# Kernel optimization log

Measured on AMD Instinct MI355X. Metric: run time of the kernel, lower is better.

The kernel has to match this reference:

```python
import jax, jax.numpy as jnp
import numpy as np

KH, KW = 3, 3
PAD = 1
STRIDE = 1


def dht1(x):
    # 1D Discrete Hartley Transform along last axis: Re(FFT) - Im(FFT)
    f = jnp.fft.fft(x, axis=-1)
    return f.real - f.imag


def dht2(x, fft_h, fft_w):
    # zero-pad trailing two dims up to (fft_h, fft_w), then DHT along w then h
    pad_h = fft_h - x.shape[-2]
    pad_w = fft_w - x.shape[-1]
    pads = [(0, 0)] * (x.ndim - 2) + [(0, pad_h), (0, pad_w)]
    x = jnp.pad(x, pads)
    x = dht1(x)
    x = jnp.swapaxes(dht1(jnp.swapaxes(x, -1, -2)), -1, -2)
    return x


def setup_inputs() -> dict:
    key = jax.random.key(0)
    k1, k2 = jax.random.split(key)
    x = jax.random.normal(k1, (8, 64, 128, 128), dtype=jnp.float32)
    weight = jax.random.normal(k2, (64, 64, KH, KW), dtype=jnp.float32)
    return {"x": x, "weight": weight}


def reference(x, weight):
    b, c_in, h, w = x.shape
    out_h = (h + 2 * PAD - KH) // STRIDE + 1
    out_w = (w + 2 * PAD - KW) // STRIDE + 1
    x_p = jnp.pad(x, ((0, 0), (0, 0), (PAD, PAD), (PAD, PAD)))
    fft_h = h + 2 * PAD + KH - 1
    fft_w = w + 2 * PAD + KW - 1

    x_ht = dht2(x_p, fft_h, fft_w)          # [B, Cin, fh, fw]
    w_ht = dht2(weight, fft_h, fft_w)        # [Cout, Cin, fh, fw]

    x_f = jnp.flip(x_ht, axis=(-2, -1))
    w_f = jnp.flip(w_ht, axis=(-2, -1))

    # Fused combine + sum over Cin: avoids [B,Cout,Cin,fh,fw] intermediates.
    t1 = jnp.einsum('bchw,ochw->bohw', x_ht, w_ht)
    t2 = jnp.einsum('bchw,ochw->bohw', x_ht, w_f)
    t3 = jnp.einsum('bchw,ochw->bohw', x_f, w_ht)
    t4 = jnp.einsum('bchw,ochw->bohw', x_f, w_f)
    out_ht = (t1 + t2 + t3 - t4) * 0.5

    # idht2 in the source applies only the 1/n scaling twice (no transform)
    output = out_ht / jnp.asarray(fft_h * fft_w, dtype=out_ht.dtype)
    return output[:, :, :out_h, :out_w]
```

## Files before the change

### kernel.cpp

```cpp
#include <hip/hip_runtime.h>
#include <hip/hip_fp16.h>


#define SCALE (0.5f / 17424.0f)

typedef __attribute__((ext_vector_type(8))) _Float16 f16x8;
typedef __attribute__((ext_vector_type(4))) _Float16 f16x4;
typedef __attribute__((ext_vector_type(4))) float    f32x4;

__global__ void build_tf16(_Float16* __restrict__ Tf) {
    const int u = blockIdx.x;
    const int i = threadIdx.x;
    float val = 0.f;
    if (u < 132) {
        const int m = (u * (i + 1)) % 132;
        const float step = 6.28318530717958647692f / 132.0f;
        float s, c;
        sincosf((float)m * step, &s, &c);
        val = c + s;
    }
    Tf[u * 128 + i] = (_Float16)val;
}

__global__ void build_cf(_Float16* __restrict__ cfT) {
    const int v = threadIdx.x;
    const float step = 6.28318530717958647692f / 132.0f;
    float s, c;
    _Float16 o[8];
    o[0] = (_Float16)1.0f; o[3] = (_Float16)1.0f;
    o[6] = (_Float16)0.0f; o[7] = (_Float16)0.0f;
    sincosf((float)((v * 1) % 132) * step, &s, &c);      o[1] = (_Float16)(c + s);
    sincosf((float)((v * 2) % 132) * step, &s, &c);      o[2] = (_Float16)(c + s);
    sincosf((float)(((v + 1) * 1) % 132) * step, &s, &c); o[4] = (_Float16)(c - s);
    sincosf((float)(((v + 1) * 2) % 132) * step, &s, &c); o[5] = (_Float16)(c - s);
    *(f16x8*)(cfT + v * 8) = *(f16x8*)o;
}

__global__ __launch_bounds__(256) void build_hgT(
    const float* __restrict__ w, _Float16* __restrict__ hgT)
{
    const int u = blockIdx.x;
    const float step = 6.28318530717958647692f / 132.0f;
    float a[3], ap[3];
    a[0] = 1.f; ap[0] = 1.f;
    #pragma unroll
    for (int i = 1; i < 3; ++i) {
        float s, c;
        sincosf((float)((u * i) % 132) * step, &s, &c);
        a[i] = c + s;
        sincosf((float)(((u + 1) * i) % 132) * step, &s, &c);
        ap[i] = c - s;
    }
    for (int it = 0; it < 16; ++it) {
        const int oc = it * 256 + threadIdx.x;
        const float* wp = w + (size_t)oc * 9;
        float w9[9];
        #pragma unroll
        for (int q = 0; q < 9; ++q) w9[q] = wp[q];
        #pragma unroll
        for (int j = 0; j < 3; ++j) {
            const float h = a[0]*w9[j] + a[1]*w9[3+j] + a[2]*w9[6+j];
            const float g = ap[0]*w9[j] + ap[1]*w9[3+j] + ap[2]*w9[6+j];
            hgT[((size_t)u * 6 + j)     * 4096 + oc] = (_Float16)h;
            hgT[((size_t)u * 6 + 3 + j) * 4096 + oc] = (_Float16)g;
        }
    }
}

__global__ __launch_bounds__(256, 2) void dht2_fused(
    const float* __restrict__ x, const _Float16* __restrict__ Tf,
    _Float16* __restrict__ X)
{
    const int bc = blockIdx.x;
    const int tid = threadIdx.x, wv = tid >> 6, lane = tid & 63;
    const int col = lane & 15, quad = lane >> 4;
    __shared__ _Float16 Tfl[144][136];
    __shared__ _Float16 Y1l[144][136];

    const float* xp = x + (size_t)bc * 16384;

    float4 xv[2][4][2];
    #pragma unroll
    for (int nt = 0; nt < 2; ++nt) {
        const int ic = (wv * 2 + nt) * 16 + col;
        #pragma unroll
        for (int kc = 0; kc < 4; ++kc) {
            const int k0 = kc * 32 + quad * 8;
            xv[nt][kc][0] = *(const float4*)(xp + ic * 128 + k0);
            xv[nt][kc][1] = *(const float4*)(xp + ic * 128 + k0 + 4);
        }
    }
    #pragma unroll
    for (int s = 0; s < 9; ++s) {
        const int idx = tid + 256 * s;
        const int row = idx >> 4;
        const int ce  = (idx & 15) * 8;
        *(f16x8*)&Tfl[row][ce] = *(const f16x8*)(Tf + (size_t)idx * 8);
    }
    f16x8 bfA[2][4];
    #pragma unroll
    for (int nt = 0; nt < 2; ++nt)
        #pragma unroll
        for (int kc = 0; kc < 4; ++kc) {
            f16x8 t;
            t[0] = (_Float16)xv[nt][kc][0].x; t[1] = (_Float16)xv[nt][kc][0].y;
            t[2] = (_Float16)xv[nt][kc][0].z; t[3] = (_Float16)xv[nt][kc][0].w;
            t[4] = (_Float16)xv[nt][kc][1].x; t[5] = (_Float16)xv[nt][kc][1].y;
            t[6] = (_Float16)xv[nt][kc][1].z; t[7] = (_Float16)xv[nt][kc][1].w;
            bfA[nt][kc] = t;
        }
    __syncthreads();

    f32x4 accA[2][9];
    #pragma unroll
    for (int nt = 0; nt < 2; ++nt)
        #pragma unroll
        for (int mt = 0; mt < 9; ++mt) accA[nt][mt] = (f32x4)0.f;
    #pragma unroll
    for (int kc = 0; kc < 4; ++kc) {
        const int k0 = kc * 32 + quad * 8;
        #pragma unroll
        for (int mt = 0; mt < 9; ++mt) {
            const f16x8 af = *(const f16x8*)&Tfl[mt * 16 + col][k0];
            accA[0][mt] = __builtin_amdgcn_mfma_f32_16x16x32_f16(af, bfA[0][kc], accA[0][mt], 0, 0, 0);
            accA[1][mt] = __builtin_amdgcn_mfma_f32_16x16x32_f16(af, bfA[1][kc], accA[1][mt], 0, 0, 0);
        }
    }
    #pragma unroll
    for (int nt = 0; nt < 2; ++nt) {
        const int ic = (wv * 2 + nt) * 16 + col;
        #pragma unroll
        for (int mt = 0; mt < 9; ++mt)
            #pragma unroll
            for (int r = 0; r < 4; ++r)
                Y1l[mt * 16 + quad * 4 + r][ic] = (_Float16)accA[nt][mt][r];
    }
    __syncthreads();

    f32x4 accB[3][9];
    #pragma unroll
    for (int t = 0; t < 3; ++t)
        #pragma unroll
        for (int mt = 0; mt < 9; ++mt) accB[t][mt] = (f32x4)0.f;
    #pragma unroll
    for (int kc = 0; kc < 4; ++kc) {
        const int k0 = kc * 32 + quad * 8;
        f16x8 af9[9];
        #pragma unroll
        for (int mt = 0; mt < 9; ++mt)
            af9[mt] = *(const f16x8*)&Tfl[mt * 16 + col][k0];
        #pragma unroll
        for (int t = 0; t < 3; ++t) {
            const int nt = wv + 4 * t;
            if (nt < 9) {
                const f16x8 bf = *(const f16x8*)&Y1l[nt * 16 + col][k0];
                #pragma unroll
                for (int mt = 0; mt < 9; ++mt)
                    accB[t][mt] = __builtin_amdgcn_mfma_f32_16x16x32_f16(af9[mt], bf, accB[t][mt], 0, 0, 0);
            }
        }
    }
    _Float16* Xp = X + (size_t)bc * 17424;
    #pragma unroll
    for (int t = 0; t < 3; ++t) {
        const int nt = wv + 4 * t;
        if (nt < 9) {
            const int vg = nt * 16 + col;
            if (vg < 132) {
                #pragma unroll
                for (int mt = 0; mt < 9; ++mt)
                    #pragma unroll
                    for (int r = 0; r < 4; ++r) {
                        const int u = mt * 16 + quad * 4 + r;
                        if (u < 132) Xp[u * 132 + vg] = (_Float16)accB[t][mt][r];
                    }
            }
        }
    }
}

__global__ __launch_bounds__(256) void combine_mfma(
    const _Float16* __restrict__ X, const _Float16* __restrict__ hgT,
    const _Float16* __restrict__ cfT, float* __restrict__ out)
{
    const int u = blockIdx.x;
    const int b = blockIdx.y;
    const int tid = threadIdx.x;
    const int wv = tid >> 6, lane = tid & 63;
    const int col = lane & 15, quad = lane >> 4;

    __shared__ _Float16 Ps[128][72];
    __shared__ _Float16 Ms[128][72];

    {
        const int c  = tid >> 2;
        const int vq = (tid & 3) * 32;
        const _Float16* rowd = X + (size_t)(b * 64 + c) * 17424 + (size_t)u * 132;
        const _Float16* rowm = X + (size_t)(b * 64 + c) * 17424 + (size_t)(131 - u) * 132;
        #pragma unroll
        for (int k = 0; k < 8; ++k) {
            const int v0 = vq + 4 * k;
            const f16x4 d = *(const f16x4*)(rowd + v0);
            const f16x4 m = *(const f16x4*)(rowm + (128 - v0));
            #pragma unroll
            for (int i = 0; i < 4; ++i) {
                Ps[v0 + i][c] = d[i] + m[3 - i];
                Ms[v0 + i][c] = d[i] - m[3 - i];
            }
        }
    }
    f16x8 cfv[8];
    #pragma unroll
    for (int nt = 0; nt < 8; ++nt)
        cfv[nt] = *(const f16x8*)(cfT + (size_t)(nt * 16 + col) * 8);
    __syncthreads();

    const _Float16* hgu = hgT + (size_t)u * 6 * 4096;
    const int orow = wv * 16 + col;
    f32x4 acc[8];
    #pragma unroll
    for (int nt = 0; nt < 8; ++nt) acc[nt] = (f32x4)0.f;

    {
        f16x8 af[6];
        #pragma unroll
        for (int ch = 0; ch < 6; ++ch) {
            const int kt = ch >> 1, c0 = (ch & 1) * 32;
            af[ch] = *(const f16x8*)(hgu + ((size_t)kt * 64 + orow) * 64 + c0 + quad * 8);
        }
        #pragma unroll
        for (int ch = 0; ch < 6; ++ch) {
            const int kt = ch >> 1, c0 = (ch & 1) * 32;
            #pragma unroll
            for (int nt = 0; nt < 8; ++nt) {
                f16x8 bf = *(const f16x8*)&Ps[nt * 16 + col][c0 + quad * 8];
                const _Float16 cs = cfv[nt][kt];
                #pragma unroll
                for (int e = 0; e < 8; ++e) bf[e] *= cs;
                acc[nt] = __builtin_amdgcn_mfma_f32_16x16x32_f16(af[ch], bf, acc[nt], 0, 0, 0);
            }
        }
    }
    {
        f16x8 af[6];
        #pragma unroll
        for (int ch = 0; ch < 6; ++ch) {
            const int kt = 3 + (ch >> 1), c0 = (ch & 1) * 32;
            af[ch] = *(const f16x8*)(hgu + ((size_t)kt * 64 + orow) * 64 + c0 + quad * 8);
        }
        #pragma unroll
        for (int ch = 0; ch < 6; ++ch) {
            const int kt = 3 + (ch >> 1), c0 = (ch & 1) * 32;
            #pragma unroll
            for (int nt = 0; nt < 8; ++nt) {
                f16x8 bf = *(const f16x8*)&Ms[nt * 16 + col][c0 + quad * 8];
                const _Float16 cs = cfv[nt][kt];
                #pragma unroll
                for (int e = 0; e < 8; ++e) bf[e] *= cs;
                acc[nt] = __builtin_amdgcn_mfma_f32_16x16x32_f16(af[ch], bf, acc[nt], 0, 0, 0);
            }
        }
    }

    #pragma unroll
    for (int nt = 0; nt < 8; ++nt) {
        const int v = nt * 16 + col;
        #pragma unroll
        for (int r = 0; r < 4; ++r) {
            const int o = wv * 16 + quad * 4 + r;
            out[(((size_t)b * 64 + o) * 128 + u) * 128 + v] = acc[nt][r] * SCALE;
        }
    }
}

extern "C" void kernel_launch(void* const* d_in, const int* in_sizes, int n_in,
                              void* d_out, int out_size, void* d_ws, size_t ws_size,
                              hipStream_t stream)
{
    const float* x = (const float*)d_in[0];
    const float* w = (const float*)d_in[1];
    char* ws = (char*)d_ws;
    _Float16* Tf  = (_Float16*)(ws);
    _Float16* cfT = (_Float16*)(ws + 36864);
    _Float16* X   = (_Float16*)(ws + 65536);
    _Float16* hgT = (_Float16*)(ws + 17907712);

    build_tf16<<<dim3(144), dim3(128), 0, stream>>>(Tf);
    build_cf<<<dim3(1), dim3(128), 0, stream>>>(cfT);

    dht2_fused<<<dim3(512), dim3(256), 0, stream>>>(x, Tf, X);

    build_hgT<<<dim3(128), dim3(256), 0, stream>>>(w, hgT);

    combine_mfma<<<dim3(128, 8), dim3(256), 0, stream>>>(
        X, hgT, cfT, (float*)d_out);
}
```

Baseline: 118.9 us.

## Pair mirrored rows in combine, merge setup kernels, stage padded X stores via LDS

The three table/weight setup kernels become one launch, with the weight transform split across more blocks. dht2_fused now stages its output in shared memory and writes X with 16-byte vector stores into a row pitch padded to 136. combine_mfma has each block compute output rows u and 131-u together, reusing the loaded H/G weight fragments and the P/M sums. This halves the number of combine blocks and weight reloads. The cost is more per-block work, a wider LDS tile and an extra barrier in dht2_fused.

```diff
diff --git a/kernel.cpp b/kernel.cpp
--- a/kernel.cpp
+++ b/kernel.cpp
@@ -3,44 +3,56 @@
 
 
 #define SCALE (0.5f / 17424.0f)
+#define MFMA  __builtin_amdgcn_mfma_f32_16x16x32_f16
 
 typedef __attribute__((ext_vector_type(8))) _Float16 f16x8;
 typedef __attribute__((ext_vector_type(4))) _Float16 f16x4;
 typedef __attribute__((ext_vector_type(4))) float    f32x4;
 
-__global__ void build_tf16(_Float16* __restrict__ Tf) {
-    const int u = blockIdx.x;
-    const int i = threadIdx.x;
-    float val = 0.f;
-    if (u < 132) {
-        const int m = (u * (i + 1)) % 132;
-        const float step = 6.28318530717958647692f / 132.0f;
-        float s, c;
-        sincosf((float)m * step, &s, &c);
-        val = c + s;
-    }
-    Tf[u * 128 + i] = (_Float16)val;
-}
-
-__global__ void build_cf(_Float16* __restrict__ cfT) {
-    const int v = threadIdx.x;
+static __device__ __forceinline__ f16x8 scl(f16x8 a, _Float16 s) {
+    #pragma unroll
+    for (int e = 0; e < 8; ++e) a[e] *= s;
+    return a;
+}
+
+__global__ __launch_bounds__(256) void build_all(
+    const float* __restrict__ w, _Float16* __restrict__ Tf,
+    _Float16* __restrict__ cfT, _Float16* __restrict__ hgT)
+{
+    const int bid = blockIdx.x;
+    const int tid = threadIdx.x;
     const float step = 6.28318530717958647692f / 132.0f;
-    float s, c;
-    _Float16 o[8];
-    o[0] = (_Float16)1.0f; o[3] = (_Float16)1.0f;
-    o[6] = (_Float16)0.0f; o[7] = (_Float16)0.0f;
-    sincosf((float)((v * 1) % 132) * step, &s, &c);      o[1] = (_Float16)(c + s);
-    sincosf((float)((v * 2) % 132) * step, &s, &c);      o[2] = (_Float16)(c + s);
-    sincosf((float)(((v + 1) * 1) % 132) * step, &s, &c); o[4] = (_Float16)(c - s);
-    sincosf((float)(((v + 1) * 2) % 132) * step, &s, &c); o[5] = (_Float16)(c - s);
-    *(f16x8*)(cfT + v * 8) = *(f16x8*)o;
-}
-
-__global__ __launch_bounds__(256) void build_hgT(
-    const float* __restrict__ w, _Float16* __restrict__ hgT)
-{
-    const int u = blockIdx.x;
-    const float step = 6.28318530717958647692f / 132.0f;
+    if (bid < 144) {
+        if (tid < 128) {
+            float val = 0.f;
+            if (bid < 132) {
+                const int m = (bid * (tid + 1)) % 132;
+                float s, c;
+                sincosf((float)m * step, &s, &c);
+                val = c + s;
+            }
+            Tf[bid * 128 + tid] = (_Float16)val;
+        }
+        return;
+    }
+    if (bid == 144) {
+        if (tid < 128) {
+            const int v = tid;
+            float s, c;
+            _Float16 o[8];
+            o[0] = (_Float16)1.0f; o[3] = (_Float16)1.0f;
+            o[6] = (_Float16)0.0f; o[7] = (_Float16)0.0f;
+            sincosf((float)((v * 1) % 132) * step, &s, &c);       o[1] = (_Float16)(c + s);
+            sincosf((float)((v * 2) % 132) * step, &s, &c);       o[2] = (_Float16)(c + s);
+            sincosf((float)(((v + 1) * 1) % 132) * step, &s, &c); o[4] = (_Float16)(c - s);
+            sincosf((float)(((v + 1) * 2) % 132) * step, &s, &c); o[5] = (_Float16)(c - s);
+            *(f16x8*)(cfT + v * 8) = *(f16x8*)o;
+        }
+        return;
+    }
+    const int bid2 = bid - 145;
+    const int u = bid2 >> 2;
+    const int itbase = (bid2 & 3) * 4;
     float a[3], ap[3];
     a[0] = 1.f; ap[0] = 1.f;
     #pragma unroll
@@ -51,8 +63,8 @@
         sincosf((float)(((u + 1) * i) % 132) * step, &s, &c);
         ap[i] = c - s;
     }
-    for (int it = 0; it < 16; ++it) {
-        const int oc = it * 256 + threadIdx.x;
+    for (int it = itbase; it < itbase + 4; ++it) {
+        const int oc = it * 256 + tid;
         const float* wp = w + (size_t)oc * 9;
         float w9[9];
         #pragma unroll
@@ -122,8 +134,8 @@
         #pragma unroll
         for (int mt = 0; mt < 9; ++mt) {
             const f16x8 af = *(const f16x8*)&Tfl[mt * 16 + col][k0];
-            accA[0][mt] = __builtin_amdgcn_mfma_f32_16x16x32_f16(af, bfA[0][kc], accA[0][mt], 0, 0, 0);
-            accA[1][mt] = __builtin_amdgcn_mfma_f32_16x16x32_f16(af, bfA[1][kc], accA[1][mt], 0, 0, 0);
+            accA[0][mt] = MFMA(af, bfA[0][kc], accA[0][mt], 0, 0, 0);
+            accA[1][mt] = MFMA(af, bfA[1][kc], accA[1][mt], 0, 0, 0);
         }
     }
     #pragma unroll
@@ -156,11 +168,12 @@
                 const f16x8 bf = *(const f16x8*)&Y1l[nt * 16 + col][k0];
                 #pragma unroll
                 for (int mt = 0; mt < 9; ++mt)
-                    accB[t][mt] = __builtin_amdgcn_mfma_f32_16x16x32_f16(af9[mt], bf, accB[t][mt], 0, 0, 0);
-            }
-        }
-    }
-    _Float16* Xp = X + (size_t)bc * 17424;
+                    accB[t][mt] = MFMA(af9[mt], bf, accB[t][mt], 0, 0, 0);
+            }
+        }
+    }
+
+    __syncthreads();
     #pragma unroll
     for (int t = 0; t < 3; ++t) {
         const int nt = wv + 4 * t;
@@ -172,9 +185,19 @@
                     #pragma unroll
                     for (int r = 0; r < 4; ++r) {
                         const int u = mt * 16 + quad * 4 + r;
-                        if (u < 132) Xp[u * 132 + vg] = (_Float16)accB[t][mt][r];
+                        if (u < 132) Tfl[u][vg] = (_Float16)accB[t][mt][r];
                     }
             }
+        }
+    }
+    __syncthreads();
+    _Float16* Xp = X + (size_t)bc * 17952;
+    #pragma unroll
+    for (int k = 0; k < 9; ++k) {
+        const int ch = tid + 256 * k;
+        if (ch < 2244) {
+            const int u = ch / 17, kk = ch - u * 17;
+            *(f16x8*)(Xp + u * 136 + kk * 8) = *(const f16x8*)&Tfl[u][kk * 8];
         }
     }
 }
@@ -183,23 +206,24 @@
     const _Float16* __restrict__ X, const _Float16* __restrict__ hgT,
     const _Float16* __restrict__ cfT, float* __restrict__ out)
 {
-    const int u = blockIdx.x;
+    const int uidx = blockIdx.x;
     const int b = blockIdx.y;
     const int tid = threadIdx.x;
     const int wv = tid >> 6, lane = tid & 63;
     const int col = lane & 15, quad = lane >> 4;
-
-    __shared__ _Float16 Ps[128][72];
-    __shared__ _Float16 Ms[128][72];
+    const int u2 = 131 - uidx;
+    const bool doB = (uidx >= 4);
+
+    __shared__ _Float16 Ps[132][72];
+    __shared__ _Float16 Ms[132][72];
 
     {
-        const int c  = tid >> 2;
-        const int vq = (tid & 3) * 32;
-        const _Float16* rowd = X + (size_t)(b * 64 + c) * 17424 + (size_t)u * 132;
-        const _Float16* rowm = X + (size_t)(b * 64 + c) * 17424 + (size_t)(131 - u) * 132;
+        const int c = tid >> 2, sub = tid & 3;
+        const _Float16* rowd = X + (size_t)(b * 64 + c) * 17952 + (size_t)uidx * 136;
+        const _Float16* rowm = X + (size_t)(b * 64 + c) * 17952 + (size_t)u2 * 136;
         #pragma unroll
         for (int k = 0; k < 8; ++k) {
-            const int v0 = vq + 4 * k;
+            const int v0 = sub * 32 + 4 * k;
             const f16x4 d = *(const f16x4*)(rowd + v0);
             const f16x4 m = *(const f16x4*)(rowm + (128 - v0));
             #pragma unroll
@@ -208,67 +232,85 @@
                 Ms[v0 + i][c] = d[i] - m[3 - i];
             }
         }
+        if (sub == 0) {
+            const f16x4 d = *(const f16x4*)(rowd + 128);
+            const f16x4 m = *(const f16x4*)(rowm);
+            #pragma unroll
+            for (int i = 0; i < 4; ++i) {
+                Ps[128 + i][c] = d[i] + m[3 - i];
+                Ms[128 + i][c] = d[i] - m[3 - i];
+            }
+        }
     }
     f16x8 cfv[8];
     #pragma unroll
     for (int nt = 0; nt < 8; ++nt)
         cfv[nt] = *(const f16x8*)(cfT + (size_t)(nt * 16 + col) * 8);
-    __syncthreads();
-
-    const _Float16* hgu = hgT + (size_t)u * 6 * 4096;
+
+    const _Float16* hgu = hgT + (size_t)uidx * 6 * 4096;
     const int orow = wv * 16 + col;
-    f32x4 acc[8];
-    #pragma unroll
-    for (int nt = 0; nt < 8; ++nt) acc[nt] = (f32x4)0.f;
-
-    {
-        f16x8 af[6];
-        #pragma unroll
-        for (int ch = 0; ch < 6; ++ch) {
-            const int kt = ch >> 1, c0 = (ch & 1) * 32;
-            af[ch] = *(const f16x8*)(hgu + ((size_t)kt * 64 + orow) * 64 + c0 + quad * 8);
-        }
-        #pragma unroll
-        for (int ch = 0; ch < 6; ++ch) {
-            const int kt = ch >> 1, c0 = (ch & 1) * 32;
-            #pragma unroll
-            for (int nt = 0; nt < 8; ++nt) {
-                f16x8 bf = *(const f16x8*)&Ps[nt * 16 + col][c0 + quad * 8];
-                const _Float16 cs = cfv[nt][kt];
-                #pragma unroll
-                for (int e = 0; e < 8; ++e) bf[e] *= cs;
-                acc[nt] = __builtin_amdgcn_mfma_f32_16x16x32_f16(af[ch], bf, acc[nt], 0, 0, 0);
-            }
-        }
-    }
-    {
-        f16x8 af[6];
-        #pragma unroll
-        for (int ch = 0; ch < 6; ++ch) {
-            const int kt = 3 + (ch >> 1), c0 = (ch & 1) * 32;
-            af[ch] = *(const f16x8*)(hgu + ((size_t)kt * 64 + orow) * 64 + c0 + quad * 8);
-        }
-        #pragma unroll
-        for (int ch = 0; ch < 6; ++ch) {
-            const int kt = 3 + (ch >> 1), c0 = (ch & 1) * 32;
-            #pragma unroll
-            for (int nt = 0; nt < 8; ++nt) {
-                f16x8 bf = *(const f16x8*)&Ms[nt * 16 + col][c0 + quad * 8];
-                const _Float16 cs = cfv[nt][kt];
-                #pragma unroll
-                for (int e = 0; e < 8; ++e) bf[e] *= cs;
-                acc[nt] = __builtin_amdgcn_mfma_f32_16x16x32_f16(af[ch], bf, acc[nt], 0, 0, 0);
-            }
-        }
-    }
+    f16x8 hA[3][2], gA[3][2];
+    #pragma unroll
+    for (int kt = 0; kt < 3; ++kt)
+        #pragma unroll
+        for (int hf = 0; hf < 2; ++hf) {
+            hA[kt][hf] = *(const f16x8*)(hgu + ((size_t)kt * 64 + orow) * 64 + hf * 32 + quad * 8);
+            gA[kt][hf] = *(const f16x8*)(hgu + ((size_t)(3 + kt) * 64 + orow) * 64 + hf * 32 + quad * 8);
+        }
+    __syncthreads();
+
+    float* outA = out + (((size_t)(b * 64 + wv * 16 + quad * 4)) * 128 + uidx) * 128 + col;
+    float* outB = out + (((size_t)(b * 64 + wv * 16 + quad * 4)) * 128 + u2) * 128 + col;
 
     #pragma unroll
     for (int nt = 0; nt < 8; ++nt) {
-        const int v = nt * 16 + col;
-        #pragma unroll
-        for (int r = 0; r < 4; ++r) {
-            const int o = wv * 16 + quad * 4 + r;
-            out[(((size_t)b * 64 + o) * 128 + u) * 128 + v] = acc[nt][r] * SCALE;
+        const int vA = nt * 16 + col;
+        const int vB = 131 - vA;
+        const _Float16 csP1 = cfv[nt][1], csP2 = cfv[nt][2];
+        const _Float16 csM1 = cfv[nt][4], csM2 = cfv[nt][5];
+        {
+            const f16x8 p0 = *(const f16x8*)&Ps[vA][quad * 8];
+            const f16x8 p1 = *(const f16x8*)&Ps[vA][32 + quad * 8];
+            const f16x8 m0 = *(const f16x8*)&Ms[vA][quad * 8];
+            const f16x8 m1 = *(const f16x8*)&Ms[vA][32 + quad * 8];
+            f32x4 aP = (f32x4)0.f, aM = (f32x4)0.f;
+            aP = MFMA(hA[0][0], p0, aP, 0, 0, 0);
+            aP = MFMA(hA[0][1], p1, aP, 0, 0, 0);
+            aM = MFMA(gA[0][0], m0, aM, 0, 0, 0);
+            aM = MFMA(gA[0][1], m1, aM, 0, 0, 0);
+            aP = MFMA(hA[1][0], scl(p0, csP1), aP, 0, 0, 0);
+            aP = MFMA(hA[1][1], scl(p1, csP1), aP, 0, 0, 0);
+            aM = MFMA(gA[1][0], scl(m0, csM1), aM, 0, 0, 0);
+            aM = MFMA(gA[1][1], scl(m1, csM1), aM, 0, 0, 0);
+            aP = MFMA(hA[2][0], scl(p0, csP2), aP, 0, 0, 0);
+            aP = MFMA(hA[2][1], scl(p1, csP2), aP, 0, 0, 0);
+            aM = MFMA(gA[2][0], scl(m0, csM2), aM, 0, 0, 0);
+            aM = MFMA(gA[2][1], scl(m1, csM2), aM, 0, 0, 0);
+            #pragma unroll
+            for (int r = 0; r < 4; ++r)
+                outA[(size_t)r * 16384 + nt * 16] = (aP[r] + aM[r]) * SCALE;
+        }
+        if (doB) {
+            const f16x8 p0 = *(const f16x8*)&Ps[vB][quad * 8];
+            const f16x8 p1 = *(const f16x8*)&Ps[vB][32 + quad * 8];
+            const f16x8 m0 = *(const f16x8*)&Ms[vB][quad * 8];
+            const f16x8 m1 = *(const f16x8*)&Ms[vB][32 + quad * 8];
+            f32x4 bP = (f32x4)0.f, bM = (f32x4)0.f;
+            bP = MFMA(gA[0][0], p0, bP, 0, 0, 0);
+            bP = MFMA(gA[0][1], p1, bP, 0, 0, 0);
+            bM = MFMA(hA[0][0], m0, bM, 0, 0, 0);
+            bM = MFMA(hA[0][1], m1, bM, 0, 0, 0);
+            bP = MFMA(gA[1][0], scl(p0, csP1), bP, 0, 0, 0);
+            bP = MFMA(gA[1][1], scl(p1, csP1), bP, 0, 0, 0);
+            bM = MFMA(hA[1][0], scl(m0, csM1), bM, 0, 0, 0);
+            bM = MFMA(hA[1][1], scl(m1, csM1), bM, 0, 0, 0);
+            bP = MFMA(gA[2][0], scl(p0, csP2), bP, 0, 0, 0);
+            bP = MFMA(gA[2][1], scl(p1, csP2), bP, 0, 0, 0);
+            bM = MFMA(hA[2][0], scl(m0, csM2), bM, 0, 0, 0);
+            bM = MFMA(hA[2][1], scl(m1, csM2), bM, 0, 0, 0);
+            #pragma unroll
+            for (int r = 0; r < 4; ++r)
+                outB[(size_t)r * 16384 + nt * 16] = (bP[r] - bM[r]) * SCALE;
         }
     }
 }
@@ -283,15 +325,12 @@
     _Float16* Tf  = (_Float16*)(ws);
     _Float16* cfT = (_Float16*)(ws + 36864);
     _Float16* X   = (_Float16*)(ws + 65536);
-    _Float16* hgT = (_Float16*)(ws + 17907712);
-
-    build_tf16<<<dim3(144), dim3(128), 0, stream>>>(Tf);
-    build_cf<<<dim3(1), dim3(128), 0, stream>>>(cfT);
+    _Float16* hgT = (_Float16*)(ws + 18448384);
+
+    build_all<<<dim3(409), dim3(256), 0, stream>>>(w, Tf, cfT, hgT);
 
     dht2_fused<<<dim3(512), dim3(256), 0, stream>>>(x, Tf, X);
 
-    build_hgT<<<dim3(128), dim3(256), 0, stream>>>(w, hgT);
-
-    combine_mfma<<<dim3(128, 8), dim3(256), 0, stream>>>(
+    combine_mfma<<<dim3(66, 8), dim3(256), 0, stream>>>(
         X, hgT, cfT, (float*)d_out);
 }
```

Result: faster. 114.4 us (-3.8%).
